# Kernel optimization log

Hardware: AMD Instinct MI355X
Metric: run time of the kernel (lower is better)

Reference implementation:

```python
import jax, jax.numpy as jnp
import numpy as np

# TTM config (matches init_kwargs)
IN_SHAPE = (15, 15, 15, 15)   # TTM_dims[0], prod = 50625 = vocab
OUT_SHAPE = (8, 8, 8, 8)      # TTM_dims[1], prod = 4096 = out_features
RANKS = (1, 32, 64, 32, 1)
ROW_DIM = IN_SHAPE[0] * IN_SHAPE[1]  # 225, first unravel axis


def setup_inputs() -> dict:
    key = jax.random.key(0)
    ks = jax.random.split(key, 5)
    import math
    order = 4
    target_sdv = 1.0
    Us = {}
    for i in range(order):
        r1, r2 = RANKS[i], RANKS[i + 1]
        n1, n2 = IN_SHAPE[i], OUT_SHAPE[i]
        Us[f"U{i}"] = (jax.random.normal(ks[i], (r1, n1, n2, r2), dtype=jnp.float32)
                        / math.sqrt(r2) * target_sdv ** (1.0 / order))
    x = jax.random.randint(ks[4], (2, 4096), 0, int(np.prod(IN_SHAPE)), dtype=jnp.int64)
    return {"x": x, **Us}


def reference(x, U0, U1, U2, U3):
    # Precompute the two merged factors (small, vocab-independent):
    # out1: (n1_0*n1_1, n2_0*n2_1, r2) ; out2: (r2, n1_2*n1_3, n2_2*n2_3)
    t1 = jnp.tensordot(U0, U1, axes=[[3], [0]])        # (1, 15, 8, 15, 8, 64)
    t1 = jnp.moveaxis(t1, 3, 2)                         # (1, 15, 15, 8, 8, 64)
    out1 = t1.reshape(IN_SHAPE[0] * IN_SHAPE[1], OUT_SHAPE[0] * OUT_SHAPE[1], RANKS[2])
    t2 = jnp.tensordot(U2, U3, axes=[[3], [0]])        # (64, 15, 8, 15, 8, 1)
    t2 = jnp.moveaxis(t2, 3, 2)                         # (64, 15, 15, 8, 8, 1)
    out2 = t2.reshape(RANKS[2], IN_SHAPE[2] * IN_SHAPE[3], OUT_SHAPE[2] * OUT_SHAPE[3])

    xshape = x.shape
    xf = x.reshape(-1)
    # unravel_index of token id over [225, 225]
    row0 = xf // ROW_DIM
    row1 = xf % ROW_DIM
    a = out1[row0]            # (B, O1, r2)
    b = out2[:, row1, :]      # (r2, B, O2)
    rows = jnp.einsum('abc,cad->abd', a, b)   # (B, O1, O2)
    rows = rows.reshape(rows.shape[0], -1)     # (B, out_features)
    return rows.reshape(*xshape, -1)           # (*x.shape, 4096)
```

## Files before the change

### kernel.cpp

```cpp
#include <hip/hip_runtime.h>
#include <hip/hip_bf16.h>
#include <stdint.h>


typedef __attribute__((ext_vector_type(8))) __bf16 bf16x8;
typedef __attribute__((ext_vector_type(4))) float f32x4;

__device__ inline unsigned short f2bf(float f) {
    union { float f; unsigned u; } v; v.f = f;
    unsigned u = v.u;
    return (unsigned short)((u + 0x7fffu + ((u >> 16) & 1u)) >> 16);
}

__global__ __launch_bounds__(256) void build_tables(const float* __restrict__ U0,
                                                    const float* __restrict__ U1,
                                                    const float* __restrict__ U2,
                                                    const float* __restrict__ U3,
                                                    unsigned short* __restrict__ O1,
                                                    unsigned short* __restrict__ O2) {
    __shared__ float smem[8960];
    const int b = blockIdx.x;
    const int t = threadIdx.x;

    f32x4 acc[4];
#pragma unroll
    for (int k = 0; k < 4; ++k) acc[k] = (f32x4){0.f, 0.f, 0.f, 0.f};

    if (b < 225) {
        float* su0 = smem;
        float* su1 = smem + 256;
        const int p = b;
        const int i0 = p / 15, i1 = p % 15;
        const int o0b = t >> 7;
        const int o1 = (t >> 4) & 7;
        const int cq = t & 15;

        su0[t] = U0[i0 * 256 + t];

        for (int h = 0; h < 2; ++h) {
            __syncthreads();
            for (int j = t; j < 8192; j += 256) {
                int r1h = j >> 9, rem = j & 511;
                su1[j] = U1[((h * 16 + r1h) * 15 + i1) * 512 + rem];
            }
            __syncthreads();
#pragma unroll
            for (int r = 0; r < 16; ++r) {
                f32x4 bvec = *(const f32x4*)(su1 + r * 512 + o1 * 64 + cq * 4);
#pragma unroll
                for (int k = 0; k < 4; ++k)
                    acc[k] += su0[(o0b + 2 * k) * 32 + h * 16 + r] * bvec;
            }
        }
#pragma unroll
        for (int k = 0; k < 4; ++k) {
            int item = t + k * 256;
            ushort4 s = { f2bf(acc[k][0]), f2bf(acc[k][1]), f2bf(acc[k][2]), f2bf(acc[k][3]) };
            *(ushort4*)(O1 + p * 4096 + item * 4) = s;
        }
    } else {
        float* su3 = smem;
        float* su2 = smem + 256;
        const int q = b - 225;
        const int i2 = q / 15, i3 = q % 15;
        const int t_lo = t & 15, t_hi = t >> 4;
        const int o2 = t_hi >> 1;
        const int o3b = (t_hi & 1) * 4;

        {
            int r3 = t >> 3, o3 = t & 7;
            su3[t] = U3[(r3 * 15 + i3) * 8 + o3];
        }

        for (int h = 0; h < 2; ++h) {
            __syncthreads();
            for (int j = t; j < 8192; j += 256) {
                int c = j >> 7, o2s = (j >> 4) & 7, r3h = j & 15;
                su2[(o2s * 16 + r3h) * 68 + c] =
                    U2[((c * 15 + i2) * 8 + o2s) * 32 + h * 16 + r3h];
            }
            __syncthreads();
#pragma unroll
            for (int r = 0; r < 16; ++r) {
                f32x4 bvec = *(const f32x4*)(su2 + (o2 * 16 + r) * 68 + t_lo * 4);
#pragma unroll
                for (int k = 0; k < 4; ++k)
                    acc[k] += su3[(h * 16 + r) * 8 + o3b + k] * bvec;
            }
        }
#pragma unroll
        for (int k = 0; k < 4; ++k) {
            int item = t_lo + k * 16 + t_hi * 64;
            ushort4 s = { f2bf(acc[k][0]), f2bf(acc[k][1]), f2bf(acc[k][2]), f2bf(acc[k][3]) };
            *(ushort4*)(O2 + q * 4096 + item * 4) = s;
        }
    }
}

__global__ __launch_bounds__(256) void ttm_main(const int* __restrict__ x,
                                                const unsigned short* __restrict__ O1,
                                                const unsigned short* __restrict__ O2,
                                                float* __restrict__ out, int ne) {
    __shared__ float lbuf[4][16 * 68];
    const int w = threadIdx.x >> 6;
    const int l = threadIdx.x & 63;
    const int e = blockIdx.x * 4 + w;
    if (e >= ne) return;

    const unsigned v = (unsigned)x[e];
    const unsigned row0 = v / 225u;
    const unsigned row1 = v - row0 * 225u;

    const int lr = l & 15;
    const int lk = l >> 4;

    const unsigned short* Yp = O1 + (size_t)row0 * 4096;
    const unsigned short* Xp = O2 + (size_t)row1 * 4096;

    bf16x8 Y[4][2], X[4][2];
#pragma unroll
    for (int mq = 0; mq < 4; ++mq)
#pragma unroll
        for (int h = 0; h < 2; ++h)
            Y[mq][h] = *(const bf16x8*)(Yp + (16 * mq + lr) * 64 + h * 32 + lk * 8);
#pragma unroll
    for (int nq = 0; nq < 4; ++nq)
#pragma unroll
        for (int h = 0; h < 2; ++h)
            X[nq][h] = *(const bf16x8*)(Xp + (16 * nq + lr) * 64 + h * 32 + lk * 8);

    float* Oe = out + (size_t)e * 4096;
    float* Lw = lbuf[w];

#pragma unroll
    for (int mq = 0; mq < 4; ++mq) {
        f32x4 acc[4];
#pragma unroll
        for (int nq = 0; nq < 4; ++nq) {
            acc[nq] = __builtin_amdgcn_mfma_f32_16x16x32_bf16(
                X[nq][0], Y[mq][0], (f32x4){0.f, 0.f, 0.f, 0.f}, 0, 0, 0);
            acc[nq] = __builtin_amdgcn_mfma_f32_16x16x32_bf16(
                X[nq][1], Y[mq][1], acc[nq], 0, 0, 0);
        }
#pragma unroll
        for (int nq = 0; nq < 4; ++nq)
            *(f32x4*)(Lw + lr * 68 + 16 * nq + 4 * lk) = acc[nq];

#pragma unroll
        for (int i = 0; i < 4; ++i) {
            int chunk = i * 64 + l;
            int row = chunk >> 4, colq = chunk & 15;
            f32x4 vv = *(const f32x4*)(Lw + row * 68 + colq * 4);
            __builtin_nontemporal_store(vv, (f32x4*)(Oe + 1024 * mq + chunk * 4));
        }
    }
}

extern "C" void kernel_launch(void* const* d_in, const int* in_sizes, int n_in,
                              void* d_out, int out_size, void* d_ws, size_t ws_size,
                              hipStream_t stream) {
    const int* x = (const int*)d_in[0];
    const float* U0 = (const float*)d_in[1];
    const float* U1 = (const float*)d_in[2];
    const float* U2 = (const float*)d_in[3];
    const float* U3 = (const float*)d_in[4];

    unsigned short* O1 = (unsigned short*)d_ws;
    unsigned short* O2 = O1 + 225 * 4096;

    const int ne = in_sizes[0];

    build_tables<<<450, 256, 0, stream>>>(U0, U1, U2, U3, O1, O2);
    ttm_main<<<(ne + 3) / 4, 256, 0, stream>>>(x, O1, O2, (float*)d_out, ne);
}
```

Measured before the change: 41.29 us.

## Switch to 32x32x16 MFMA and store accumulators directly without LDS staging

The per-token 64x64 product now uses 32x32x16 bf16 MFMA tiles instead of 16x16x32. This changes the operand fragment layout and the number of MFMA instructions. The LDS transpose buffer is removed, and each accumulator element is written straight to global memory with scalar nontemporal stores, so lanes write contiguous 32-float row segments. This drops LDS traffic and shared memory use but replaces 128-bit stores with 32-bit stores, which may reduce store efficiency in this output-bandwidth-bound kernel.

```diff
diff --git a/kernel.cpp b/kernel.cpp
--- a/kernel.cpp
+++ b/kernel.cpp
@@ -5,6 +5,7 @@
 
 typedef __attribute__((ext_vector_type(8))) __bf16 bf16x8;
 typedef __attribute__((ext_vector_type(4))) float f32x4;
+typedef __attribute__((ext_vector_type(16))) float f32x16;
 
 __device__ inline unsigned short f2bf(float f) {
     union { float f; unsigned u; } v; v.f = f;
@@ -101,7 +102,6 @@
                                                 const unsigned short* __restrict__ O1,
                                                 const unsigned short* __restrict__ O2,
                                                 float* __restrict__ out, int ne) {
-    __shared__ float lbuf[4][16 * 68];
     const int w = threadIdx.x >> 6;
     const int l = threadIdx.x & 63;
     const int e = blockIdx.x * 4 + w;
@@ -111,47 +111,41 @@
     const unsigned row0 = v / 225u;
     const unsigned row1 = v - row0 * 225u;
 
-    const int lr = l & 15;
-    const int lk = l >> 4;
+    const int lr = l & 31;
+    const int lh = l >> 5;
 
-    const unsigned short* Yp = O1 + (size_t)row0 * 4096;
-    const unsigned short* Xp = O2 + (size_t)row1 * 4096;
+    const unsigned short* Ap = O1 + (size_t)row0 * 4096;
+    const unsigned short* Bp = O2 + (size_t)row1 * 4096;
 
-    bf16x8 Y[4][2], X[4][2];
+    bf16x8 B[2][4];
 #pragma unroll
-    for (int mq = 0; mq < 4; ++mq)
+    for (int nh = 0; nh < 2; ++nh)
 #pragma unroll
-        for (int h = 0; h < 2; ++h)
-            Y[mq][h] = *(const bf16x8*)(Yp + (16 * mq + lr) * 64 + h * 32 + lk * 8);
-#pragma unroll
-    for (int nq = 0; nq < 4; ++nq)
-#pragma unroll
-        for (int h = 0; h < 2; ++h)
-            X[nq][h] = *(const bf16x8*)(Xp + (16 * nq + lr) * 64 + h * 32 + lk * 8);
+        for (int kk = 0; kk < 4; ++kk)
+            B[nh][kk] = *(const bf16x8*)(Bp + (32 * nh + lr) * 64 + kk * 16 + lh * 8);
 
     float* Oe = out + (size_t)e * 4096;
-    float* Lw = lbuf[w];
 
 #pragma unroll
-    for (int mq = 0; mq < 4; ++mq) {
-        f32x4 acc[4];
+    for (int mh = 0; mh < 2; ++mh) {
+        bf16x8 A[4];
 #pragma unroll
-        for (int nq = 0; nq < 4; ++nq) {
-            acc[nq] = __builtin_amdgcn_mfma_f32_16x16x32_bf16(
-                X[nq][0], Y[mq][0], (f32x4){0.f, 0.f, 0.f, 0.f}, 0, 0, 0);
-            acc[nq] = __builtin_amdgcn_mfma_f32_16x16x32_bf16(
-                X[nq][1], Y[mq][1], acc[nq], 0, 0, 0);
-        }
-#pragma unroll
-        for (int nq = 0; nq < 4; ++nq)
-            *(f32x4*)(Lw + lr * 68 + 16 * nq + 4 * lk) = acc[nq];
+        for (int kk = 0; kk < 4; ++kk)
+            A[kk] = *(const bf16x8*)(Ap + (32 * mh + lr) * 64 + kk * 16 + lh * 8);
 
 #pragma unroll
-        for (int i = 0; i < 4; ++i) {
-            int chunk = i * 64 + l;
-            int row = chunk >> 4, colq = chunk & 15;
-            f32x4 vv = *(const f32x4*)(Lw + row * 68 + colq * 4);
-            __builtin_nontemporal_store(vv, (f32x4*)(Oe + 1024 * mq + chunk * 4));
+        for (int nh = 0; nh < 2; ++nh) {
+            f32x16 acc = {0.f, 0.f, 0.f, 0.f, 0.f, 0.f, 0.f, 0.f,
+                          0.f, 0.f, 0.f, 0.f, 0.f, 0.f, 0.f, 0.f};
+#pragma unroll
+            for (int kk = 0; kk < 4; ++kk)
+                acc = __builtin_amdgcn_mfma_f32_32x32x16_bf16(A[kk], B[nh][kk], acc, 0, 0, 0);
+
+#pragma unroll
+            for (int i = 0; i < 16; ++i) {
+                int row = 32 * mh + (i & 3) + 8 * (i >> 2) + 4 * lh;
+                __builtin_nontemporal_store(acc[i], Oe + row * 64 + 32 * nh + lr);
+            }
         }
     }
 }
```

Result: slower. 43.18 us (+4.6%).
